# Performance work log

Measured on AMD Instinct MI355X. Metric: run time of the kernel, lower is better.

Reference implementation:

```python
import jax, jax.numpy as jnp
import numpy as np

# Straight-through spike with triangular surrogate gradient (matches SpikeFunction)
@jax.custom_vjp
def spike(v_scaled):
    return (v_scaled > 0).astype(v_scaled.dtype)

def _spike_fwd(v_scaled):
    return spike(v_scaled), v_scaled

def _spike_bwd(v_scaled, g):
    return (g * jnp.clip(1.0 - jnp.abs(v_scaled), 0.0, None),)

spike.defvjp(_spike_fwd, _spike_bwd)

_SIGMOID_H = np.array([-0.11408895, 1.1758447, 1.0135335, 1.2213913, 1.3241712, 0.8555309, 1.4268297, 1.1778928, 0.80728793, 0.43790972, 0.2571573, 0.13942857, -0.3750314, 0.08095932, 1.354895, 5.0583024], dtype=np.float32)
_SIGMOID_D = np.array([1.1759424, 1.0134453, 1.221452, 1.3243698, 0.85503244, 1.4270093, 1.1782365, 0.8076809, 0.43830687, 0.2571347, 0.13936771, -0.04276754, 0.07785574, 0.05046117, 0.10240205, 0.02330057], dtype=np.float32)
_SIGMOID_T = np.array([1.3393638, 1.3052133, 1.3697962, 1.3982388, 1.264561, 1.3956275, 1.1693456, 0.79711413, 0.42847168, 0.24717589, 0.13019533, 0.52669114, 0.06617433, 0.0366448, 1.0000271, 0.01022558], dtype=np.float32)

def setup_inputs() -> dict:
    key = jax.random.key(0)
    x = jax.random.normal(key, (8, 2048, 4096), dtype=jnp.float32)
    return {
        "x": x,
        "h": jnp.asarray(_SIGMOID_H),
        "d": jnp.asarray(_SIGMOID_D),
        "T": jnp.asarray(_SIGMOID_T),
    }

def reference(x, h, d, T):
    # fast=True path of FsCoding10.forward
    signs = jax.lax.stop_gradient(jnp.sign(x))
    x_abs = jnp.abs(x)

    def step(carry, hdT):
        v, z, out = carry
        ht, dt, Tt = hdT
        v = v - z * ht
        v_scaled = (v - Tt) / (jnp.abs(v) + 1.0)
        z = spike(v_scaled)
        out = out + z * dt
        return (v, z, out), None

    init = (x_abs, jnp.zeros_like(x_abs), jnp.zeros_like(x_abs))
    (_, _, out), _ = jax.lax.scan(step, init, (h, d, T))  # K=16 steps
    return out * signs
```

## Files before the change

### kernel.cpp

```cpp
#include <hip/hip_runtime.h>


#define NTHREADS 256
#define NBLOCKS  8192

typedef float f32x2 __attribute__((ext_vector_type(2)));
typedef float f32x4 __attribute__((ext_vector_type(4)));

__device__ __forceinline__ f32x2 fs10_pair(f32x2 xi) {
    constexpr float H[16] = {
        -0.11408895f, 1.1758447f, 1.0135335f, 1.2213913f,
         1.3241712f,  0.8555309f, 1.4268297f, 1.1778928f,
         0.80728793f, 0.43790972f, 0.2571573f, 0.13942857f,
        -0.3750314f,  0.08095932f, 1.354895f,  5.0583024f};
    constexpr float D[16] = {
         1.1759424f,  1.0134453f, 1.221452f,  1.3243698f,
         0.85503244f, 1.4270093f, 1.1782365f, 0.8076809f,
         0.43830687f, 0.2571347f, 0.13936771f, -0.04276754f,
         0.07785574f, 0.05046117f, 0.10240205f, 0.02330057f};
    constexpr float T[16] = {
         1.3393638f,  1.3052133f, 1.3697962f, 1.3982388f,
         1.264561f,   1.3956275f, 1.1693456f, 0.79711413f,
         0.42847168f, 0.24717589f, 0.13019533f, 0.52669114f,
         0.06617433f, 0.0366448f, 1.0000271f, 0.01022558f};

    f32x2 v, z, a;
    v.x = fabsf(xi.x);
    v.y = fabsf(xi.y);
    z.x = (v.x > T[0]) ? 1.0f : 0.0f;
    z.y = (v.y > T[0]) ? 1.0f : 0.0f;
    a.x = z.x * D[0];
    a.y = z.y * D[0];
#pragma unroll
    for (int t = 1; t < 16; ++t) {
        const f32x2 nh = {-H[t], -H[t]};
        const f32x2 dd = { D[t],  D[t]};
        v = __builtin_elementwise_fma(z, nh, v);
        z.x = (v.x > T[t]) ? 1.0f : 0.0f;
        z.y = (v.y > T[t]) ? 1.0f : 0.0f;
        a = __builtin_elementwise_fma(z, dd, a);
    }
    f32x2 r;
    r.x = copysignf(a.x, xi.x);
    r.y = copysignf(a.y, xi.y);
    return r;
}

__device__ __forceinline__ f32x4 fs10_quad(f32x4 xv) {
    f32x2 lo = {xv.x, xv.y}, hi = {xv.z, xv.w};
    f32x2 rlo = fs10_pair(lo), rhi = fs10_pair(hi);
    f32x4 r;
    r.x = rlo.x; r.y = rlo.y; r.z = rhi.x; r.w = rhi.y;
    return r;
}

__global__ __launch_bounds__(NTHREADS)
void fs10_kernel(const f32x4* __restrict__ x, f32x4* __restrict__ out,
                 int n4, const float* __restrict__ xs, float* __restrict__ outs,
                 int n) {
    const int stride = gridDim.x * blockDim.x;
    int i = blockIdx.x * blockDim.x + threadIdx.x;

    for (; i + stride < n4; i += 2 * stride) {
        f32x4 xa = __builtin_nontemporal_load(&x[i]);
        f32x4 xb = __builtin_nontemporal_load(&x[i + stride]);
        f32x4 ra = fs10_quad(xa);
        f32x4 rb = fs10_quad(xb);
        __builtin_nontemporal_store(ra, &out[i]);
        __builtin_nontemporal_store(rb, &out[i + stride]);
    }
    for (; i < n4; i += stride) {
        f32x4 xv = __builtin_nontemporal_load(&x[i]);
        __builtin_nontemporal_store(fs10_quad(xv), &out[i]);
    }
    const int tail_base = n4 << 2;
    for (int j = tail_base + blockIdx.x * blockDim.x + threadIdx.x; j < n;
         j += stride) {
        f32x2 p = {xs[j], 0.0f};
        outs[j] = fs10_pair(p).x;
    }
}

extern "C" void kernel_launch(void* const* d_in, const int* in_sizes, int n_in,
                              void* d_out, int out_size, void* d_ws, size_t ws_size,
                              hipStream_t stream) {
    const float* x = (const float*)d_in[0];
    float* out     = (float*)d_out;
    const int n    = in_sizes[0];
    const int n4   = n >> 2;

    int blocks = (n4 + NTHREADS - 1) / NTHREADS;
    if (blocks > NBLOCKS) blocks = NBLOCKS;
    if (blocks < 1) blocks = 1;

    fs10_kernel<<<blocks, NTHREADS, 0, stream>>>(
        (const f32x4*)x, (f32x4*)out, n4, x, out, n);
}
```

Before: 107.1 us.

## Replace grid-stride loop with one-element-per-thread launch and separate tail kernel

Removes the block cap and grid-stride loop so each thread processes a single float4, launching enough blocks to cover the whole array. The scalar tail handling moves into its own small kernel launched only when the element count is not a multiple of four. This aims to cut loop overhead and simplify scheduling, at the cost of more blocks and fewer loads in flight per thread.

```diff
diff --git a/kernel.cpp b/kernel.cpp
--- a/kernel.cpp
+++ b/kernel.cpp
@@ -2,7 +2,6 @@
 
 
 #define NTHREADS 256
-#define NBLOCKS  8192
 
 typedef float f32x2 __attribute__((ext_vector_type(2)));
 typedef float f32x4 __attribute__((ext_vector_type(4)));
@@ -55,29 +54,21 @@
 }
 
 __global__ __launch_bounds__(NTHREADS)
-void fs10_kernel(const f32x4* __restrict__ x, f32x4* __restrict__ out,
-                 int n4, const float* __restrict__ xs, float* __restrict__ outs,
-                 int n) {
-    const int stride = gridDim.x * blockDim.x;
-    int i = blockIdx.x * blockDim.x + threadIdx.x;
-
-    for (; i + stride < n4; i += 2 * stride) {
-        f32x4 xa = __builtin_nontemporal_load(&x[i]);
-        f32x4 xb = __builtin_nontemporal_load(&x[i + stride]);
-        f32x4 ra = fs10_quad(xa);
-        f32x4 rb = fs10_quad(xb);
-        __builtin_nontemporal_store(ra, &out[i]);
-        __builtin_nontemporal_store(rb, &out[i + stride]);
-    }
-    for (; i < n4; i += stride) {
+void fs10_kernel(const f32x4* __restrict__ x, f32x4* __restrict__ out, int n4) {
+    const int i = blockIdx.x * NTHREADS + threadIdx.x;
+    if (i < n4) {
         f32x4 xv = __builtin_nontemporal_load(&x[i]);
         __builtin_nontemporal_store(fs10_quad(xv), &out[i]);
     }
-    const int tail_base = n4 << 2;
-    for (int j = tail_base + blockIdx.x * blockDim.x + threadIdx.x; j < n;
-         j += stride) {
-        f32x2 p = {xs[j], 0.0f};
-        outs[j] = fs10_pair(p).x;
+}
+
+__global__ __launch_bounds__(64)
+void fs10_tail(const float* __restrict__ x, float* __restrict__ out,
+               int start, int n) {
+    const int i = start + blockIdx.x * 64 + threadIdx.x;
+    if (i < n) {
+        f32x2 p = {x[i], 0.0f};
+        out[i] = fs10_pair(p).x;
     }
 }
 
@@ -89,10 +80,13 @@
     const int n    = in_sizes[0];
     const int n4   = n >> 2;
 
-    int blocks = (n4 + NTHREADS - 1) / NTHREADS;
-    if (blocks > NBLOCKS) blocks = NBLOCKS;
-    if (blocks < 1) blocks = 1;
-
-    fs10_kernel<<<blocks, NTHREADS, 0, stream>>>(
-        (const f32x4*)x, (f32x4*)out, n4, x, out, n);
+    if (n4 > 0) {
+        const int blocks = (n4 + NTHREADS - 1) / NTHREADS;
+        fs10_kernel<<<blocks, NTHREADS, 0, stream>>>(
+            (const f32x4*)x, (f32x4*)out, n4);
+    }
+    const int tail = n - (n4 << 2);
+    if (tail > 0) {
+        fs10_tail<<<(tail + 63) / 64, 64, 0, stream>>>(x, out, n4 << 2, n);
+    }
 }
```

New measurement: 108.6 us. Within noise of the previous version (+1.4%).
